# Optimization experiments

Hardware: AMD Instinct MI355X
Metric: run time of the kernel (lower is better)

Reference implementation:

```python
import jax, jax.numpy as jnp
import numpy as np

DIM = 2048
N_HEADS = 16
Q_LORA = 1536
KV_LORA = 512
NOPE = 128
ROPE = 64
V_DIM = 128
B, T = 1, 3072
EPS = 1e-6


def rmsnorm(x, w):
    var = jnp.mean(jnp.square(x), axis=-1, keepdims=True)
    return x * jax.lax.rsqrt(var + EPS) * w


def apply_rope(x, cos, sin):
    # x: (B, T, H, d); cos/sin: (T, d//2) -> broadcast (1, T, 1, d//2)
    c = cos[None, :, None, :]
    s = sin[None, :, None, :]
    x1 = x[..., 0::2]
    x2 = x[..., 1::2]
    r1 = x1 * c - x2 * s
    r2 = x1 * s + x2 * c
    return jnp.stack([r1, r2], axis=-1).reshape(x.shape)


def setup_inputs() -> dict:
    key = jax.random.key(0)
    ks = jax.random.split(key, 10)
    std = 0.02
    x = jax.random.normal(ks[0], (B, T, DIM), dtype=jnp.float32)
    # RoPE angles: position * inv_freq, shape (T, ROPE//2)
    inv_freq = 1.0 / (10000.0 ** (np.arange(0, ROPE, 2, dtype=np.float32) / ROPE))
    freqs = jnp.asarray(np.arange(T, dtype=np.float32)[:, None] * inv_freq[None, :])
    # additive causal mask (T, T)
    mask = jnp.where(jnp.tril(jnp.ones((T, T), dtype=bool)), 0.0, -jnp.inf).astype(jnp.float32)
    wq_down = jax.random.normal(ks[1], (DIM, Q_LORA), dtype=jnp.float32) * std
    q_norm_w = jnp.ones((Q_LORA,), dtype=jnp.float32)
    wq_nope = jax.random.normal(ks[2], (Q_LORA, N_HEADS * NOPE), dtype=jnp.float32) * std
    wq_rope = jax.random.normal(ks[3], (Q_LORA, N_HEADS * ROPE), dtype=jnp.float32) * std
    wkv_down = jax.random.normal(ks[4], (DIM, KV_LORA + ROPE), dtype=jnp.float32) * std
    kv_norm_w = jnp.ones((KV_LORA,), dtype=jnp.float32)
    wkv_up = jax.random.normal(ks[5], (KV_LORA, N_HEADS * (NOPE + V_DIM)), dtype=jnp.float32) * std
    wo = jax.random.normal(ks[6], (N_HEADS * V_DIM, DIM), dtype=jnp.float32) * std
    return {
        'x': x, 'freqs': freqs, 'mask': mask,
        'wq_down': wq_down, 'q_norm_w': q_norm_w, 'wq_nope': wq_nope,
        'wq_rope': wq_rope, 'wkv_down': wkv_down, 'kv_norm_w': kv_norm_w,
        'wkv_up': wkv_up, 'wo': wo,
    }


def reference(x, freqs, mask, wq_down, q_norm_w, wq_nope, wq_rope,
              wkv_down, kv_norm_w, wkv_up, wo):
    cos, sin = jnp.cos(freqs), jnp.sin(freqs)
    # Q path: down-project, RMSNorm, split nope/rope heads
    q_lat = rmsnorm(x @ wq_down, q_norm_w)                      # (B,T,Q_LORA)
    q_nope = (q_lat @ wq_nope).reshape(B, T, N_HEADS, NOPE)
    q_rope = apply_rope((q_lat @ wq_rope).reshape(B, T, N_HEADS, ROPE), cos, sin)
    q = jnp.concatenate([q_nope, q_rope], axis=-1)              # (B,T,H,192)
    # KV path: joint down-projection -> latent c_kv + raw rope key
    kvd = x @ wkv_down                                          # (B,T,KV_LORA+ROPE)
    c_kv = kvd[..., :KV_LORA]
    k_rope_raw = kvd[..., KV_LORA:]                             # (B,T,ROPE)
    k_rope = jnp.broadcast_to(k_rope_raw[:, :, None, :], (B, T, N_HEADS, ROPE))
    k_rope = apply_rope(k_rope, cos, sin)
    kv_up = (rmsnorm(c_kv, kv_norm_w) @ wkv_up).reshape(B, T, N_HEADS, NOPE + V_DIM)
    k_nope = kv_up[..., :NOPE]
    v = kv_up[..., NOPE:]                                       # (B,T,H,V_DIM)
    k = jnp.concatenate([k_nope, k_rope], axis=-1)              # (B,T,H,192)
    scale = (NOPE + ROPE) ** (-0.5)
    attn = jnp.einsum('bqhd,bkhd->bhqk', q, k) * scale + mask[None, None]
    attn = jax.nn.softmax(attn, axis=-1)                        # dropout p=0 (eval)
    out = jnp.einsum('bhqk,bkhd->bqhd', attn, v).reshape(B, T, N_HEADS * V_DIM)
    return out @ wo                                             # (B,T,DIM)
```

## Files before the change

### kernel.cpp

```cpp
#include <hip/hip_runtime.h>
#include <hip/hip_bf16.h>

typedef __bf16 bf16_t;
typedef __bf16 bf16x8 __attribute__((ext_vector_type(8)));
typedef float f32x4 __attribute__((ext_vector_type(4)));

#define T_SEQ 3072
#define DIM 2048
#define NH 16
#define QLORA 1536
#define KVLORA 512
#define NOPE 128
#define ROPE 64
#define VDIM 128
#define HD 192
#define SCALE 0.07216878364870323f
#define CHUNK 12

#define T1KV_LD 2112
#define QNR_LD 3072

__device__ inline float wave_reduce_sum(float v) {
    #pragma unroll
    for (int off = 32; off > 0; off >>= 1) v += __shfl_down(v, off);
    return v;
}

__device__ inline float block_reduce_sum_256(float v) {
    __shared__ float red[4];
    int lane = threadIdx.x & 63, w = threadIdx.x >> 6;
    v = wave_reduce_sum(v);
    if (lane == 0) red[w] = v;
    __syncthreads();
    if (threadIdx.x == 0) red[0] = red[0] + red[1] + red[2] + red[3];
    __syncthreads();
    return red[0];
}

__device__ inline void glds16(const bf16_t* g, bf16_t* l) {
    __builtin_amdgcn_global_load_lds(
        (const __attribute__((address_space(1))) unsigned int*)g,
        (__attribute__((address_space(3))) unsigned int*)l, 16, 0, 0);
}

__global__ void f2b_kernel(const float* __restrict__ in, bf16_t* __restrict__ out, int n) {
    int i = (blockIdx.x * 256 + threadIdx.x) * 4;
    if (i < n) {
        float4 v = *(const float4*)&in[i];
        bf16_t o[4] = {(bf16_t)v.x, (bf16_t)v.y, (bf16_t)v.z, (bf16_t)v.w};
        *(uint2*)&out[i] = *(const uint2*)o;
    }
}

__global__ __launch_bounds__(256) void transp_kernel(
    const float* __restrict__ in, bf16_t* __restrict__ out, int K, int N)
{
    __shared__ float tile[32][33];
    int k0 = blockIdx.y * 32, n0 = blockIdx.x * 32;
    int tx = threadIdx.x & 31, ty = threadIdx.x >> 5;
    #pragma unroll
    for (int i = 0; i < 4; ++i)
        tile[ty + i * 8][tx] = in[(size_t)(k0 + ty + i * 8) * N + n0 + tx];
    __syncthreads();
    #pragma unroll
    for (int i = 0; i < 4; ++i)
        out[(size_t)(n0 + ty + i * 8) * K + k0 + tx] = (bf16_t)tile[tx][ty + i * 8];
}

__global__ __launch_bounds__(256) void vt_transp(
    const bf16_t* __restrict__ kvu, bf16_t* __restrict__ vt)
{
    __shared__ bf16_t tile[32][34];
    int t0 = blockIdx.x * 32, d0 = blockIdx.y * 32, h = blockIdx.z;
    int tx = threadIdx.x & 31, ty = threadIdx.x >> 5;
    #pragma unroll
    for (int i = 0; i < 4; ++i)
        tile[ty + i * 8][tx] = kvu[(size_t)(t0 + ty + i * 8) * (NH * 256) + h * 256 + NOPE + d0 + tx];
    __syncthreads();
    #pragma unroll
    for (int i = 0; i < 4; ++i)
        vt[((size_t)h * VDIM + d0 + ty + i * 8) * T_SEQ + t0 + tx] = tile[tx][ty + i * 8];
}

__global__ __launch_bounds__(256) void gemm_mfma(
    const bf16_t* __restrict__ A, const bf16_t* __restrict__ Bt,
    float* __restrict__ Cf, bf16_t* __restrict__ Cb,
    int M, int N, int K, int lda, int ldb, int ldc, int writef)
{
    __shared__ __align__(16) bf16_t As[2][128 * 32];
    __shared__ __align__(16) bf16_t Bs[2][128 * 32];
    int tid = threadIdx.x;
    int w = tid >> 6, lane = tid & 63;
    int quad = lane >> 4, l16 = lane & 15;
    int bm = blockIdx.y * 128, bn = blockIdx.x * 128;
    int wm = (w & 1) * 64, wn = (w >> 1) * 64;

    int srow = tid >> 2, soff = (tid & 3) * 8;
    const bf16_t* a0 = A + (size_t)(bm + srow) * lda + soff;
    const bf16_t* a1 = A + (size_t)(bm + 64 + srow) * lda + soff;
    int br0 = bn + srow;      if (br0 >= N) br0 = N - 1;
    int br1 = bn + 64 + srow; if (br1 >= N) br1 = N - 1;
    const bf16_t* b0 = Bt + (size_t)br0 * ldb + soff;
    const bf16_t* b1 = Bt + (size_t)br1 * ldb + soff;

    f32x4 acc[4][4];
    #pragma unroll
    for (int i = 0; i < 4; ++i)
        #pragma unroll
        for (int j = 0; j < 4; ++j)
            acc[i][j] = (f32x4){0.f, 0.f, 0.f, 0.f};

    int nk = K >> 5;
    glds16(a0, &As[0][tid * 8]);
    glds16(a1, &As[0][tid * 8 + 2048]);
    glds16(b0, &Bs[0][tid * 8]);
    glds16(b1, &Bs[0][tid * 8 + 2048]);
    a0 += 32; a1 += 32; b0 += 32; b1 += 32;

    for (int t = 0; t < nk; ++t) {
        int cur = t & 1;
        if (t + 1 < nk) {
            int nxt = cur ^ 1;
            glds16(a0, &As[nxt][tid * 8]);
            glds16(a1, &As[nxt][tid * 8 + 2048]);
            glds16(b0, &Bs[nxt][tid * 8]);
            glds16(b1, &Bs[nxt][tid * 8 + 2048]);
            a0 += 32; a1 += 32; b0 += 32; b1 += 32;
            asm volatile("s_waitcnt vmcnt(4)" ::: "memory");
        } else {
            asm volatile("s_waitcnt vmcnt(0)" ::: "memory");
        }
        __builtin_amdgcn_s_barrier();
        __builtin_amdgcn_sched_barrier(0);

        bf16x8 af[4], bfr[4];
        #pragma unroll
        for (int t4 = 0; t4 < 4; ++t4) {
            af[t4]  = *(const bf16x8*)&As[cur][(wm + t4 * 16 + l16) * 32 + quad * 8];
            bfr[t4] = *(const bf16x8*)&Bs[cur][(wn + t4 * 16 + l16) * 32 + quad * 8];
        }
        #pragma unroll
        for (int i = 0; i < 4; ++i)
            #pragma unroll
            for (int j = 0; j < 4; ++j)
                acc[i][j] = __builtin_amdgcn_mfma_f32_16x16x32_bf16(af[i], bfr[j], acc[i][j], 0, 0, 0);

        __builtin_amdgcn_sched_barrier(0);
        __builtin_amdgcn_s_barrier();
    }

    #pragma unroll
    for (int i = 0; i < 4; ++i) {
        #pragma unroll
        for (int j = 0; j < 4; ++j) {
            #pragma unroll
            for (int r = 0; r < 4; ++r) {
                int row = bm + wm + i * 16 + quad * 4 + r;
                int col = bn + wn + j * 16 + l16;
                if (col < N) {
                    if (writef) Cf[(size_t)row * ldc + col] = acc[i][j][r];
                    else        Cb[(size_t)row * ldc + col] = (bf16_t)acc[i][j][r];
                }
            }
        }
    }
}

__global__ __launch_bounds__(256) void rmsnorm_rows(
    bf16_t* __restrict__ X, const float* __restrict__ w, int N, int ld)
{
    int row = blockIdx.x;
    bf16_t* x = X + (size_t)row * ld;
    float ss = 0.f;
    for (int i = threadIdx.x; i < N; i += 256) { float v = (float)x[i]; ss += v * v; }
    ss = block_reduce_sum_256(ss);
    float sc = rsqrtf(ss / (float)N + 1e-6f);
    for (int i = threadIdx.x; i < N; i += 256)
        x[i] = (bf16_t)((float)x[i] * sc * w[i]);
}

__global__ __launch_bounds__(256) void kv_post(
    const bf16_t* __restrict__ kvd, const float* __restrict__ w,
    const float* __restrict__ freqs,
    bf16_t* __restrict__ ckvn, bf16_t* __restrict__ kr)
{
    int row = blockIdx.x;
    const bf16_t* src = kvd + (size_t)row * T1KV_LD;
    float ss = 0.f;
    for (int i = threadIdx.x; i < KVLORA; i += 256) { float v = (float)src[i]; ss += v * v; }
    ss = block_reduce_sum_256(ss);
    float sc = rsqrtf(ss / (float)KVLORA + 1e-6f);
    for (int i = threadIdx.x; i < KVLORA; i += 256)
        ckvn[(size_t)row * KVLORA + i] = (bf16_t)((float)src[i] * sc * w[i]);
    if (threadIdx.x < 32) {
        int i = threadIdx.x;
        float f = freqs[row * 32 + i];
        float c = cosf(f), s = sinf(f);
        float x1 = (float)src[KVLORA + 2 * i], x2 = (float)src[KVLORA + 2 * i + 1];
        kr[(size_t)row * ROPE + 2 * i]     = (bf16_t)(x1 * c - x2 * s);
        kr[(size_t)row * ROPE + 2 * i + 1] = (bf16_t)(x1 * s + x2 * c);
    }
}

__global__ void rope_q(bf16_t* __restrict__ qr, const float* __restrict__ freqs) {
    int idx = blockIdx.x * 256 + threadIdx.x;
    if (idx >= T_SEQ * NH * 32) return;
    int t = idx >> 9;
    int rem = idx & 511;
    int h = rem >> 5;
    int i = rem & 31;
    float f = freqs[t * 32 + i];
    float c = cosf(f), s = sinf(f);
    bf16_t* p = qr + (size_t)t * QNR_LD + h * ROPE + 2 * i;
    float x1 = (float)p[0], x2 = (float)p[1];
    p[0] = (bf16_t)(x1 * c - x2 * s);
    p[1] = (bf16_t)(x1 * s + x2 * c);
}

#define P_STRIDE 72
__device__ inline int slot_base(int qt, int h) {
    int b = qt / CHUNK;
    return h * 120 + qt + 6 * b * (b - 1) + (qt - CHUNK * b) * b;
}
__global__ __launch_bounds__(256) void attn_v8(
    const bf16_t* __restrict__ QNR,
    const bf16_t* __restrict__ KVU, const bf16_t* __restrict__ KR,
    const bf16_t* __restrict__ Vt,
    bf16_t* __restrict__ Opart, float* __restrict__ lpart)
{
    __shared__ __align__(16) bf16_t Kn[64 * 128];
    __shared__ __align__(16) bf16_t Kr[64 * 64];
    __shared__ __align__(16) bf16_t Vs[128 * 64];
    __shared__ __align__(16) bf16_t Ps[4][16 * P_STRIDE];

    int qt = blockIdx.x, cx = blockIdx.y, h = blockIdx.z;
    if (cx > qt / CHUNK) return;
    int slot = slot_base(qt, h) + cx;
    int kt0 = cx * CHUNK;
    int kt1 = min(qt + 1, kt0 + CHUNK);

    int tid = threadIdx.x;
    int w = tid >> 6, lane = tid & 63;
    int quad = lane >> 4, l16 = lane & 15;
    int qbase = qt * 64;

    bf16x8 qf[6];
    {
        int qrow = qbase + w * 16 + l16;
        #pragma unroll
        for (int kk = 0; kk < 4; ++kk)
            qf[kk] = *(const bf16x8*)&QNR[(size_t)qrow * QNR_LD + h * NOPE + kk * 32 + quad * 8];
        #pragma unroll
        for (int kk = 4; kk < 6; ++kk)
            qf[kk] = *(const bf16x8*)&QNR[(size_t)qrow * QNR_LD + (NH * NOPE) + h * ROPE + (kk - 4) * 32 + quad * 8];
    }

    int l4 = lane >> 4, l3 = lane >> 3;
    const bf16_t* kn_e = KVU + (size_t)(kt0 * 64 + w * 16 + l4) * (NH * 256) + h * 256 + ((lane & 15) ^ l4) * 8;
    const bf16_t* kn_o = KVU + (size_t)(kt0 * 64 + w * 16 + l4) * (NH * 256) + h * 256 + ((lane & 15) ^ (4 + l4)) * 8;
    const bf16_t* krp  = KR  + (size_t)(kt0 * 64 + w * 16 + l3) * ROPE + ((lane & 7) ^ l3) * 8;
    const bf16_t* vp   = Vt  + ((size_t)h * VDIM + w * 32 + l3) * T_SEQ + kt0 * 64 + ((lane & 7) ^ l3) * 8;

    bf16x8 ones;
    #pragma unroll
    for (int i = 0; i < 8; ++i) ones[i] = (bf16_t)1.0f;

    f32x4 o[8];
    #pragma unroll
    for (int nt = 0; nt < 8; ++nt) o[nt] = (f32x4){0.f, 0.f, 0.f, 0.f};
    f32x4 lacc = (f32x4){0.f, 0.f, 0.f, 0.f};

    for (int kt = kt0; kt < kt1; ++kt) {
        int kbase = kt * 64;
        #pragma unroll
        for (int i = 0; i < 4; ++i)
            glds16(((i & 1) ? kn_o : kn_e) + (size_t)i * 4 * (NH * 256), &Kn[(w * 4 + i) * 512]);
        #pragma unroll
        for (int i = 0; i < 2; ++i)
            glds16(krp + (size_t)i * 8 * ROPE, &Kr[(w * 2 + i) * 512]);
        #pragma unroll
        for (int i = 0; i < 4; ++i)
            glds16(vp + (size_t)i * 8 * T_SEQ, &Vs[(w * 4 + i) * 512]);
        kn_e += (size_t)64 * NH * 256;
        kn_o += (size_t)64 * NH * 256;
        krp  += 64 * ROPE;
        vp   += 64;
        __syncthreads();

        f32x4 S[4];
        #pragma unroll
        for (int c = 0; c < 4; ++c) S[c] = (f32x4){0.f, 0.f, 0.f, 0.f};
        #pragma unroll
        for (int kk = 0; kk < 4; ++kk) {
            #pragma unroll
            for (int c = 0; c < 4; ++c) {
                bf16x8 kf = *(const bf16x8*)&Kn[(c * 16 + l16) * 128 + (((kk * 4 + quad) ^ (l16 & 7)) * 8)];
                S[c] = __builtin_amdgcn_mfma_f32_16x16x32_bf16(qf[kk], kf, S[c], 0, 0, 0);
            }
        }
        #pragma unroll
        for (int kk = 4; kk < 6; ++kk) {
            #pragma unroll
            for (int c = 0; c < 4; ++c) {
                bf16x8 kf = *(const bf16x8*)&Kr[(c * 16 + l16) * 64 + ((((kk - 4) * 4 + quad) ^ (l16 & 7)) * 8)];
                S[c] = __builtin_amdgcn_mfma_f32_16x16x32_bf16(qf[kk], kf, S[c], 0, 0, 0);
            }
        }

        #pragma unroll
        for (int c = 0; c < 4; ++c) {
            #pragma unroll
            for (int j = 0; j < 4; ++j) {
                int col = kbase + c * 16 + l16;
                int grow = qbase + w * 16 + quad * 4 + j;
                float p = (col <= grow) ? __expf(S[c][j] * SCALE) : 0.f;
                Ps[w][(quad * 4 + j) * P_STRIDE + c * 16 + l16] = (bf16_t)p;
            }
        }
        __asm__ volatile("s_waitcnt lgkmcnt(0)" ::: "memory");

        bf16x8 pf0 = *(const bf16x8*)&Ps[w][l16 * P_STRIDE + quad * 8];
        bf16x8 pf1 = *(const bf16x8*)&Ps[w][l16 * P_STRIDE + 32 + quad * 8];
        lacc = __builtin_amdgcn_mfma_f32_16x16x32_bf16(pf0, ones, lacc, 0, 0, 0);
        lacc = __builtin_amdgcn_mfma_f32_16x16x32_bf16(pf1, ones, lacc, 0, 0, 0);

        #pragma unroll
        for (int kk2 = 0; kk2 < 2; ++kk2) {
            bf16x8 pf = kk2 ? pf1 : pf0;
            #pragma unroll
            for (int nt = 0; nt < 8; ++nt) {
                bf16x8 vf = *(const bf16x8*)&Vs[(nt * 16 + l16) * 64 + (((kk2 * 4 + quad) ^ (l16 & 7)) * 8)];
                o[nt] = __builtin_amdgcn_mfma_f32_16x16x32_bf16(pf, vf, o[nt], 0, 0, 0);
            }
        }
        __syncthreads();
    }

    #pragma unroll
    for (int nt = 0; nt < 8; ++nt)
        #pragma unroll
        for (int j = 0; j < 4; ++j)
            Opart[(size_t)slot * 8192 + (w * 16 + quad * 4 + j) * 128 + nt * 16 + l16] = (bf16_t)o[nt][j];
    if (l16 == 0) {
        #pragma unroll
        for (int j = 0; j < 4; ++j)
            lpart[slot * 64 + w * 16 + quad * 4 + j] = lacc[j];
    }
}

__global__ __launch_bounds__(256) void attn_combine(
    const bf16_t* __restrict__ Opart, const float* __restrict__ lpart,
    bf16_t* __restrict__ AO)
{
    int qt = blockIdx.x, h = blockIdx.y;
    int nch = qt / CHUNK + 1;
    int base = slot_base(qt, h);
    int r = threadIdx.x >> 2, c0 = (threadIdx.x & 3) * 32;

    float acc[32];
    #pragma unroll
    for (int i = 0; i < 32; ++i) acc[i] = 0.f;
    float lsum = 0.f;
    for (int ch = 0; ch < nch; ++ch) {
        int slot = base + ch;
        const bf16_t* p = &Opart[(size_t)slot * 8192 + r * 128 + c0];
        #pragma unroll
        for (int v = 0; v < 4; ++v) {
            bf16x8 u = *(const bf16x8*)&p[v * 8];
            #pragma unroll
            for (int e = 0; e < 8; ++e) acc[v * 8 + e] += (float)u[e];
        }
        lsum += lpart[slot * 64 + r];
    }
    float inv = 1.0f / lsum;
    bf16_t* dst = AO + (size_t)(qt * 64 + r) * (NH * VDIM) + h * VDIM + c0;
    #pragma unroll
    for (int v = 0; v < 4; ++v) {
        bf16_t tmp[8];
        #pragma unroll
        for (int e = 0; e < 8; ++e) tmp[e] = (bf16_t)(acc[v * 8 + e] * inv);
        *(uint4*)&dst[v * 8] = *(const uint4*)tmp;
    }
}

extern "C" void kernel_launch(void* const* d_in, const int* in_sizes, int n_in,
                              void* d_out, int out_size, void* d_ws, size_t ws_size,
                              hipStream_t stream) {
    const float* x        = (const float*)d_in[0];
    const float* freqs    = (const float*)d_in[1];
    const float* wq_down  = (const float*)d_in[3];
    const float* q_norm_w = (const float*)d_in[4];
    const float* wq_nope  = (const float*)d_in[5];
    const float* wq_rope  = (const float*)d_in[6];
    const float* wkv_down = (const float*)d_in[7];
    const float* kv_norm_w= (const float*)d_in[8];
    const float* wkv_up   = (const float*)d_in[9];
    const float* wo       = (const float*)d_in[10];
    float* out = (float*)d_out;

    bf16_t* ws = (bf16_t*)d_ws;
    bf16_t* xb     = ws;
    bf16_t* wqd_t  = xb     + 6291456;
    bf16_t* wkvd_t = wqd_t  + 3145728;
    bf16_t* wqn_t  = wkvd_t + 1179648;
    bf16_t* wqr_t  = wqn_t  + 3145728;
    bf16_t* wkvu_t = wqr_t  + 1572864;
    bf16_t* t1kv   = wkvu_t + 2097152;
    bf16_t* ckvn   = t1kv   + 6488064;
    bf16_t* Opart  = ws;
    float*  lpart  = (float*)(ws + 15728640);
    bf16_t* ao     = ws + 15728640 + 245760;
    bf16_t* wo_t   = ws    + 25493504;
    bf16_t* kr     = wo_t  + 4194304;
    bf16_t* qnr    = kr    + 196608;
    bf16_t* kvu    = qnr   + 9437184;
    bf16_t* vt     = kvu   + 12582912;

    f2b_kernel<<<T_SEQ * DIM / 4 / 256, 256, 0, stream>>>(x, xb, T_SEQ * DIM);
    transp_kernel<<<dim3(QLORA / 32, DIM / 32), 256, 0, stream>>>(wq_down, wqd_t, DIM, QLORA);
    transp_kernel<<<dim3((KVLORA + ROPE) / 32, DIM / 32), 256, 0, stream>>>(wkv_down, wkvd_t, DIM, KVLORA + ROPE);
    transp_kernel<<<dim3(NH * NOPE / 32, QLORA / 32), 256, 0, stream>>>(wq_nope, wqn_t, QLORA, NH * NOPE);
    transp_kernel<<<dim3(NH * ROPE / 32, QLORA / 32), 256, 0, stream>>>(wq_rope, wqr_t, QLORA, NH * ROPE);
    transp_kernel<<<dim3(NH * 256 / 32, KVLORA / 32), 256, 0, stream>>>(wkv_up, wkvu_t, KVLORA, NH * 256);
    transp_kernel<<<dim3(DIM / 32, DIM / 32), 256, 0, stream>>>(wo, wo_t, DIM, DIM);

    gemm_mfma<<<dim3(17, T_SEQ / 128), 256, 0, stream>>>(
        xb, wqd_t, nullptr, t1kv, T_SEQ, 2112, DIM, DIM, DIM, T1KV_LD, 0);

    rmsnorm_rows<<<T_SEQ, 256, 0, stream>>>(t1kv, q_norm_w, QLORA, T1KV_LD);
    kv_post<<<T_SEQ, 256, 0, stream>>>(t1kv + QLORA, kv_norm_w, freqs, ckvn, kr);

    gemm_mfma<<<dim3(24, T_SEQ / 128), 256, 0, stream>>>(
        t1kv, wqn_t, nullptr, qnr, T_SEQ, 3072, QLORA, T1KV_LD, QLORA, QNR_LD, 0);
    rope_q<<<(T_SEQ * NH * 32 + 255) / 256, 256, 0, stream>>>(qnr + NH * NOPE, freqs);

    gemm_mfma<<<dim3(NH * 256 / 128, T_SEQ / 128), 256, 0, stream>>>(
        ckvn, wkvu_t, nullptr, kvu, T_SEQ, NH * 256, KVLORA, KVLORA, KVLORA, NH * 256, 0);

    vt_transp<<<dim3(T_SEQ / 32, VDIM / 32, NH), 256, 0, stream>>>(kvu, vt);

    attn_v8<<<dim3(T_SEQ / 64, 4, NH), 256, 0, stream>>>(qnr, kvu, kr, vt, Opart, lpart);
    attn_combine<<<dim3(T_SEQ / 64, NH), 256, 0, stream>>>(Opart, lpart, ao);

    gemm_mfma<<<dim3(DIM / 128, T_SEQ / 128), 256, 0, stream>>>(
        ao, wo_t, out, nullptr, T_SEQ, DIM, DIM, DIM, DIM, DIM, 1);
}
```

Baseline: 476.8 us.

## Double query tile per attention block and double-buffer K/V loads

The split-K attention kernel now uses 512 threads and covers 128 query rows per block instead of 64. Each loaded K/V tile therefore serves twice as many queries, which halves global K/V traffic. K, rope-K and V tiles are double-buffered in LDS, and the next tile's async global-to-LDS loads are issued before computing on the current tile, with explicit vmcnt waits. Slot indexing and the combine kernel are adjusted for the new tile and chunk layout. The trade-off is doubled LDS use, fewer blocks, and more masked-out work per diagonal tile.

```diff
diff --git a/kernel.cpp b/kernel.cpp
--- a/kernel.cpp
+++ b/kernel.cpp
@@ -147,6 +147,7 @@
 
         __builtin_amdgcn_sched_barrier(0);
         __builtin_amdgcn_s_barrier();
+        __builtin_amdgcn_sched_barrier(0);
     }
 
     #pragma unroll
@@ -218,31 +219,29 @@
 }
 
 #define P_STRIDE 72
-__device__ inline int slot_base(int qt, int h) {
-    int b = qt / CHUNK;
-    return h * 120 + qt + 6 * b * (b - 1) + (qt - CHUNK * b) * b;
-}
-__global__ __launch_bounds__(256) void attn_v8(
+__global__ __launch_bounds__(512) void attn_v9(
     const bf16_t* __restrict__ QNR,
     const bf16_t* __restrict__ KVU, const bf16_t* __restrict__ KR,
     const bf16_t* __restrict__ Vt,
     bf16_t* __restrict__ Opart, float* __restrict__ lpart)
 {
-    __shared__ __align__(16) bf16_t Kn[64 * 128];
-    __shared__ __align__(16) bf16_t Kr[64 * 64];
-    __shared__ __align__(16) bf16_t Vs[128 * 64];
-    __shared__ __align__(16) bf16_t Ps[4][16 * P_STRIDE];
-
-    int qt = blockIdx.x, cx = blockIdx.y, h = blockIdx.z;
-    if (cx > qt / CHUNK) return;
-    int slot = slot_base(qt, h) + cx;
+    __shared__ __align__(16) bf16_t Kn[2][64 * 128];
+    __shared__ __align__(16) bf16_t Kr[2][64 * 64];
+    __shared__ __align__(16) bf16_t Vs[2][128 * 64];
+    __shared__ __align__(16) bf16_t Ps[8][16 * P_STRIDE];
+
+    int qt2 = blockIdx.x, cx = blockIdx.y, h = blockIdx.z;
+    int ktmax = 2 * qt2 + 2;
     int kt0 = cx * CHUNK;
-    int kt1 = min(qt + 1, kt0 + CHUNK);
+    if (kt0 >= ktmax) return;
+    int kt1 = min(ktmax, kt0 + CHUNK);
+    int g = qt2 / 6, r6 = qt2 - g * 6;
+    int slot = h * 60 + 3 * g * (g + 1) + r6 * (g + 1) + cx;
 
     int tid = threadIdx.x;
     int w = tid >> 6, lane = tid & 63;
     int quad = lane >> 4, l16 = lane & 15;
-    int qbase = qt * 64;
+    int qbase = qt2 * 128;
 
     bf16x8 qf[6];
     {
@@ -256,10 +255,10 @@
     }
 
     int l4 = lane >> 4, l3 = lane >> 3;
-    const bf16_t* kn_e = KVU + (size_t)(kt0 * 64 + w * 16 + l4) * (NH * 256) + h * 256 + ((lane & 15) ^ l4) * 8;
-    const bf16_t* kn_o = KVU + (size_t)(kt0 * 64 + w * 16 + l4) * (NH * 256) + h * 256 + ((lane & 15) ^ (4 + l4)) * 8;
-    const bf16_t* krp  = KR  + (size_t)(kt0 * 64 + w * 16 + l3) * ROPE + ((lane & 7) ^ l3) * 8;
-    const bf16_t* vp   = Vt  + ((size_t)h * VDIM + w * 32 + l3) * T_SEQ + kt0 * 64 + ((lane & 7) ^ l3) * 8;
+    const bf16_t* kn0 = KVU + (size_t)(kt0 * 64 + w * 8 + l4) * (NH * 256) + h * 256 + ((lane & 15) ^ l4) * 8;
+    const bf16_t* kn1 = KVU + (size_t)(kt0 * 64 + w * 8 + 4 + l4) * (NH * 256) + h * 256 + ((lane & 15) ^ (4 + l4)) * 8;
+    const bf16_t* krp = KR + (size_t)(kt0 * 64 + w * 8 + l3) * ROPE + ((lane & 7) ^ l3) * 8;
+    const bf16_t* vp  = Vt + ((size_t)h * VDIM + w * 16 + l3) * T_SEQ + kt0 * 64 + ((lane & 7) ^ l3) * 8;
 
     bf16x8 ones;
     #pragma unroll
@@ -270,22 +269,32 @@
     for (int nt = 0; nt < 8; ++nt) o[nt] = (f32x4){0.f, 0.f, 0.f, 0.f};
     f32x4 lacc = (f32x4){0.f, 0.f, 0.f, 0.f};
 
+    glds16(kn0,               &Kn[0][w * 1024]);
+    glds16(kn1,               &Kn[0][w * 1024 + 512]);
+    glds16(krp,               &Kr[0][w * 512]);
+    glds16(vp,                &Vs[0][w * 1024]);
+    glds16(vp + 8 * T_SEQ,    &Vs[0][w * 1024 + 512]);
+    kn0 += (size_t)64 * NH * 256; kn1 += (size_t)64 * NH * 256;
+    krp += 64 * ROPE; vp += 64;
+
     for (int kt = kt0; kt < kt1; ++kt) {
         int kbase = kt * 64;
-        #pragma unroll
-        for (int i = 0; i < 4; ++i)
-            glds16(((i & 1) ? kn_o : kn_e) + (size_t)i * 4 * (NH * 256), &Kn[(w * 4 + i) * 512]);
-        #pragma unroll
-        for (int i = 0; i < 2; ++i)
-            glds16(krp + (size_t)i * 8 * ROPE, &Kr[(w * 2 + i) * 512]);
-        #pragma unroll
-        for (int i = 0; i < 4; ++i)
-            glds16(vp + (size_t)i * 8 * T_SEQ, &Vs[(w * 4 + i) * 512]);
-        kn_e += (size_t)64 * NH * 256;
-        kn_o += (size_t)64 * NH * 256;
-        krp  += 64 * ROPE;
-        vp   += 64;
-        __syncthreads();
+        int cur = (kt - kt0) & 1;
+        if (kt + 1 < kt1) {
+            int nxt = cur ^ 1;
+            glds16(kn0,            &Kn[nxt][w * 1024]);
+            glds16(kn1,            &Kn[nxt][w * 1024 + 512]);
+            glds16(krp,            &Kr[nxt][w * 512]);
+            glds16(vp,             &Vs[nxt][w * 1024]);
+            glds16(vp + 8 * T_SEQ, &Vs[nxt][w * 1024 + 512]);
+            kn0 += (size_t)64 * NH * 256; kn1 += (size_t)64 * NH * 256;
+            krp += 64 * ROPE; vp += 64;
+            asm volatile("s_waitcnt vmcnt(5)" ::: "memory");
+        } else {
+            asm volatile("s_waitcnt vmcnt(0)" ::: "memory");
+        }
+        __builtin_amdgcn_s_barrier();
+        __builtin_amdgcn_sched_barrier(0);
 
         f32x4 S[4];
         #pragma unroll
@@ -294,7 +303,7 @@
         for (int kk = 0; kk < 4; ++kk) {
             #pragma unroll
             for (int c = 0; c < 4; ++c) {
-                bf16x8 kf = *(const bf16x8*)&Kn[(c * 16 + l16) * 128 + (((kk * 4 + quad) ^ (l16 & 7)) * 8)];
+                bf16x8 kf = *(const bf16x8*)&Kn[cur][(c * 16 + l16) * 128 + (((kk * 4 + quad) ^ (l16 & 7)) * 8)];
                 S[c] = __builtin_amdgcn_mfma_f32_16x16x32_bf16(qf[kk], kf, S[c], 0, 0, 0);
             }
         }
@@ -302,7 +311,7 @@
         for (int kk = 4; kk < 6; ++kk) {
             #pragma unroll
             for (int c = 0; c < 4; ++c) {
-                bf16x8 kf = *(const bf16x8*)&Kr[(c * 16 + l16) * 64 + ((((kk - 4) * 4 + quad) ^ (l16 & 7)) * 8)];
+                bf16x8 kf = *(const bf16x8*)&Kr[cur][(c * 16 + l16) * 64 + ((((kk - 4) * 4 + quad) ^ (l16 & 7)) * 8)];
                 S[c] = __builtin_amdgcn_mfma_f32_16x16x32_bf16(qf[kk], kf, S[c], 0, 0, 0);
             }
         }
@@ -329,32 +338,35 @@
             bf16x8 pf = kk2 ? pf1 : pf0;
             #pragma unroll
             for (int nt = 0; nt < 8; ++nt) {
-                bf16x8 vf = *(const bf16x8*)&Vs[(nt * 16 + l16) * 64 + (((kk2 * 4 + quad) ^ (l16 & 7)) * 8)];
+                bf16x8 vf = *(const bf16x8*)&Vs[cur][(nt * 16 + l16) * 64 + (((kk2 * 4 + quad) ^ (l16 & 7)) * 8)];
                 o[nt] = __builtin_amdgcn_mfma_f32_16x16x32_bf16(pf, vf, o[nt], 0, 0, 0);
             }
         }
-        __syncthreads();
+        __builtin_amdgcn_sched_barrier(0);
+        __builtin_amdgcn_s_barrier();
+        __builtin_amdgcn_sched_barrier(0);
     }
 
     #pragma unroll
     for (int nt = 0; nt < 8; ++nt)
         #pragma unroll
         for (int j = 0; j < 4; ++j)
-            Opart[(size_t)slot * 8192 + (w * 16 + quad * 4 + j) * 128 + nt * 16 + l16] = (bf16_t)o[nt][j];
+            Opart[(size_t)slot * 16384 + (w * 16 + quad * 4 + j) * 128 + nt * 16 + l16] = (bf16_t)o[nt][j];
     if (l16 == 0) {
         #pragma unroll
         for (int j = 0; j < 4; ++j)
-            lpart[slot * 64 + w * 16 + quad * 4 + j] = lacc[j];
-    }
-}
-
-__global__ __launch_bounds__(256) void attn_combine(
+            lpart[slot * 128 + w * 16 + quad * 4 + j] = lacc[j];
+    }
+}
+
+__global__ __launch_bounds__(512) void attn_combine(
     const bf16_t* __restrict__ Opart, const float* __restrict__ lpart,
     bf16_t* __restrict__ AO)
 {
-    int qt = blockIdx.x, h = blockIdx.y;
-    int nch = qt / CHUNK + 1;
-    int base = slot_base(qt, h);
+    int qt2 = blockIdx.x, h = blockIdx.y;
+    int g = qt2 / 6, r6 = qt2 - g * 6;
+    int nch = g + 1;
+    int base = h * 60 + 3 * g * (g + 1) + r6 * (g + 1);
     int r = threadIdx.x >> 2, c0 = (threadIdx.x & 3) * 32;
 
     float acc[32];
@@ -363,17 +375,17 @@
     float lsum = 0.f;
     for (int ch = 0; ch < nch; ++ch) {
         int slot = base + ch;
-        const bf16_t* p = &Opart[(size_t)slot * 8192 + r * 128 + c0];
+        const bf16_t* p = &Opart[(size_t)slot * 16384 + r * 128 + c0];
         #pragma unroll
         for (int v = 0; v < 4; ++v) {
             bf16x8 u = *(const bf16x8*)&p[v * 8];
             #pragma unroll
             for (int e = 0; e < 8; ++e) acc[v * 8 + e] += (float)u[e];
         }
-        lsum += lpart[slot * 64 + r];
+        lsum += lpart[slot * 128 + r];
     }
     float inv = 1.0f / lsum;
-    bf16_t* dst = AO + (size_t)(qt * 64 + r) * (NH * VDIM) + h * VDIM + c0;
+    bf16_t* dst = AO + (size_t)(qt2 * 128 + r) * (NH * VDIM) + h * VDIM + c0;
     #pragma unroll
     for (int v = 0; v < 4; ++v) {
         bf16_t tmp[8];
@@ -439,8 +451,8 @@
 
     vt_transp<<<dim3(T_SEQ / 32, VDIM / 32, NH), 256, 0, stream>>>(kvu, vt);
 
-    attn_v8<<<dim3(T_SEQ / 64, 4, NH), 256, 0, stream>>>(qnr, kvu, kr, vt, Opart, lpart);
-    attn_combine<<<dim3(T_SEQ / 64, NH), 256, 0, stream>>>(Opart, lpart, ao);
+    attn_v9<<<dim3(T_SEQ / 128, 4, NH), 512, 0, stream>>>(qnr, kvu, kr, vt, Opart, lpart);
+    attn_combine<<<dim3(T_SEQ / 128, NH), 512, 0, stream>>>(Opart, lpart, ao);
 
     gemm_mfma<<<dim3(DIM / 128, T_SEQ / 128), 256, 0, stream>>>(
         ao, wo_t, out, nullptr, T_SEQ, DIM, DIM, DIM, DIM, DIM, 1);
```

Result: slower. 529.1 us (+11.0%).

## Process two query tiles per attention block to reuse K/V tiles

Applied to the files above, without the earlier changes.

The attention kernel now handles 128 query rows per block, as two 64-row sub-tiles sharing each loaded K and V tile, which halves global-to-LDS K/V traffic per query. Slot indexing, partial buffers and the combine kernel are reworked for 128-row slots, and the combine now uses 512 threads. The cost is double the accumulator and Q-fragment registers, bounded by launch_bounds(256,2), and fewer blocks for the causal split. A sched_barrier is also added after the GEMM loop barrier.

```diff
diff --git a/kernel.cpp b/kernel.cpp
--- a/kernel.cpp
+++ b/kernel.cpp
@@ -147,6 +147,7 @@
 
         __builtin_amdgcn_sched_barrier(0);
         __builtin_amdgcn_s_barrier();
+        __builtin_amdgcn_sched_barrier(0);
     }
 
     #pragma unroll
@@ -218,11 +219,7 @@
 }
 
 #define P_STRIDE 72
-__device__ inline int slot_base(int qt, int h) {
-    int b = qt / CHUNK;
-    return h * 120 + qt + 6 * b * (b - 1) + (qt - CHUNK * b) * b;
-}
-__global__ __launch_bounds__(256) void attn_v8(
+__global__ __launch_bounds__(256, 2) void attn_v10(
     const bf16_t* __restrict__ QNR,
     const bf16_t* __restrict__ KVU, const bf16_t* __restrict__ KR,
     const bf16_t* __restrict__ Vt,
@@ -231,28 +228,31 @@
     __shared__ __align__(16) bf16_t Kn[64 * 128];
     __shared__ __align__(16) bf16_t Kr[64 * 64];
     __shared__ __align__(16) bf16_t Vs[128 * 64];
-    __shared__ __align__(16) bf16_t Ps[4][16 * P_STRIDE];
-
-    int qt = blockIdx.x, cx = blockIdx.y, h = blockIdx.z;
-    if (cx > qt / CHUNK) return;
-    int slot = slot_base(qt, h) + cx;
+    __shared__ __align__(16) bf16_t Ps[4][32 * P_STRIDE];
+
+    int qt2 = blockIdx.x, cx = blockIdx.y, h = blockIdx.z;
+    int ktmax = 2 * qt2 + 2;
     int kt0 = cx * CHUNK;
-    int kt1 = min(qt + 1, kt0 + CHUNK);
+    if (kt0 >= ktmax) return;
+    int kt1 = min(ktmax, kt0 + CHUNK);
+    int g = qt2 / 6, r6 = qt2 - g * 6;
+    int slot = h * 60 + 3 * g * (g + 1) + r6 * (g + 1) + cx;
 
     int tid = threadIdx.x;
     int w = tid >> 6, lane = tid & 63;
     int quad = lane >> 4, l16 = lane & 15;
-    int qbase = qt * 64;
-
-    bf16x8 qf[6];
-    {
-        int qrow = qbase + w * 16 + l16;
+    int qbase = qt2 * 128;
+
+    bf16x8 qf[2][6];
+    #pragma unroll
+    for (int qs = 0; qs < 2; ++qs) {
+        int qrow = qbase + qs * 64 + w * 16 + l16;
         #pragma unroll
         for (int kk = 0; kk < 4; ++kk)
-            qf[kk] = *(const bf16x8*)&QNR[(size_t)qrow * QNR_LD + h * NOPE + kk * 32 + quad * 8];
+            qf[qs][kk] = *(const bf16x8*)&QNR[(size_t)qrow * QNR_LD + h * NOPE + kk * 32 + quad * 8];
         #pragma unroll
         for (int kk = 4; kk < 6; ++kk)
-            qf[kk] = *(const bf16x8*)&QNR[(size_t)qrow * QNR_LD + (NH * NOPE) + h * ROPE + (kk - 4) * 32 + quad * 8];
+            qf[qs][kk] = *(const bf16x8*)&QNR[(size_t)qrow * QNR_LD + (NH * NOPE) + h * ROPE + (kk - 4) * 32 + quad * 8];
     }
 
     int l4 = lane >> 4, l3 = lane >> 3;
@@ -265,10 +265,14 @@
     #pragma unroll
     for (int i = 0; i < 8; ++i) ones[i] = (bf16_t)1.0f;
 
-    f32x4 o[8];
-    #pragma unroll
-    for (int nt = 0; nt < 8; ++nt) o[nt] = (f32x4){0.f, 0.f, 0.f, 0.f};
-    f32x4 lacc = (f32x4){0.f, 0.f, 0.f, 0.f};
+    f32x4 o[2][8];
+    #pragma unroll
+    for (int qs = 0; qs < 2; ++qs)
+        #pragma unroll
+        for (int nt = 0; nt < 8; ++nt) o[qs][nt] = (f32x4){0.f, 0.f, 0.f, 0.f};
+    f32x4 lacc[2];
+    lacc[0] = (f32x4){0.f, 0.f, 0.f, 0.f};
+    lacc[1] = (f32x4){0.f, 0.f, 0.f, 0.f};
 
     for (int kt = kt0; kt < kt1; ++kt) {
         int kbase = kt * 64;
@@ -287,15 +291,18 @@
         vp   += 64;
         __syncthreads();
 
-        f32x4 S[4];
-        #pragma unroll
-        for (int c = 0; c < 4; ++c) S[c] = (f32x4){0.f, 0.f, 0.f, 0.f};
+        f32x4 S[2][4];
+        #pragma unroll
+        for (int qs = 0; qs < 2; ++qs)
+            #pragma unroll
+            for (int c = 0; c < 4; ++c) S[qs][c] = (f32x4){0.f, 0.f, 0.f, 0.f};
         #pragma unroll
         for (int kk = 0; kk < 4; ++kk) {
             #pragma unroll
             for (int c = 0; c < 4; ++c) {
                 bf16x8 kf = *(const bf16x8*)&Kn[(c * 16 + l16) * 128 + (((kk * 4 + quad) ^ (l16 & 7)) * 8)];
-                S[c] = __builtin_amdgcn_mfma_f32_16x16x32_bf16(qf[kk], kf, S[c], 0, 0, 0);
+                S[0][c] = __builtin_amdgcn_mfma_f32_16x16x32_bf16(qf[0][kk], kf, S[0][c], 0, 0, 0);
+                S[1][c] = __builtin_amdgcn_mfma_f32_16x16x32_bf16(qf[1][kk], kf, S[1][c], 0, 0, 0);
             }
         }
         #pragma unroll
@@ -303,58 +310,70 @@
             #pragma unroll
             for (int c = 0; c < 4; ++c) {
                 bf16x8 kf = *(const bf16x8*)&Kr[(c * 16 + l16) * 64 + ((((kk - 4) * 4 + quad) ^ (l16 & 7)) * 8)];
-                S[c] = __builtin_amdgcn_mfma_f32_16x16x32_bf16(qf[kk], kf, S[c], 0, 0, 0);
+                S[0][c] = __builtin_amdgcn_mfma_f32_16x16x32_bf16(qf[0][kk], kf, S[0][c], 0, 0, 0);
+                S[1][c] = __builtin_amdgcn_mfma_f32_16x16x32_bf16(qf[1][kk], kf, S[1][c], 0, 0, 0);
             }
         }
 
         #pragma unroll
-        for (int c = 0; c < 4; ++c) {
-            #pragma unroll
-            for (int j = 0; j < 4; ++j) {
-                int col = kbase + c * 16 + l16;
-                int grow = qbase + w * 16 + quad * 4 + j;
-                float p = (col <= grow) ? __expf(S[c][j] * SCALE) : 0.f;
-                Ps[w][(quad * 4 + j) * P_STRIDE + c * 16 + l16] = (bf16_t)p;
+        for (int qs = 0; qs < 2; ++qs) {
+            #pragma unroll
+            for (int c = 0; c < 4; ++c) {
+                #pragma unroll
+                for (int j = 0; j < 4; ++j) {
+                    int col = kbase + c * 16 + l16;
+                    int grow = qbase + qs * 64 + w * 16 + quad * 4 + j;
+                    float p = (col <= grow) ? __expf(S[qs][c][j] * SCALE) : 0.f;
+                    Ps[w][(qs * 16 + quad * 4 + j) * P_STRIDE + c * 16 + l16] = (bf16_t)p;
+                }
             }
         }
         __asm__ volatile("s_waitcnt lgkmcnt(0)" ::: "memory");
 
-        bf16x8 pf0 = *(const bf16x8*)&Ps[w][l16 * P_STRIDE + quad * 8];
-        bf16x8 pf1 = *(const bf16x8*)&Ps[w][l16 * P_STRIDE + 32 + quad * 8];
-        lacc = __builtin_amdgcn_mfma_f32_16x16x32_bf16(pf0, ones, lacc, 0, 0, 0);
-        lacc = __builtin_amdgcn_mfma_f32_16x16x32_bf16(pf1, ones, lacc, 0, 0, 0);
+        bf16x8 pf[2][2];
+        #pragma unroll
+        for (int qs = 0; qs < 2; ++qs) {
+            pf[qs][0] = *(const bf16x8*)&Ps[w][(qs * 16 + l16) * P_STRIDE + quad * 8];
+            pf[qs][1] = *(const bf16x8*)&Ps[w][(qs * 16 + l16) * P_STRIDE + 32 + quad * 8];
+            lacc[qs] = __builtin_amdgcn_mfma_f32_16x16x32_bf16(pf[qs][0], ones, lacc[qs], 0, 0, 0);
+            lacc[qs] = __builtin_amdgcn_mfma_f32_16x16x32_bf16(pf[qs][1], ones, lacc[qs], 0, 0, 0);
+        }
 
         #pragma unroll
         for (int kk2 = 0; kk2 < 2; ++kk2) {
-            bf16x8 pf = kk2 ? pf1 : pf0;
             #pragma unroll
             for (int nt = 0; nt < 8; ++nt) {
                 bf16x8 vf = *(const bf16x8*)&Vs[(nt * 16 + l16) * 64 + (((kk2 * 4 + quad) ^ (l16 & 7)) * 8)];
-                o[nt] = __builtin_amdgcn_mfma_f32_16x16x32_bf16(pf, vf, o[nt], 0, 0, 0);
+                o[0][nt] = __builtin_amdgcn_mfma_f32_16x16x32_bf16(pf[0][kk2], vf, o[0][nt], 0, 0, 0);
+                o[1][nt] = __builtin_amdgcn_mfma_f32_16x16x32_bf16(pf[1][kk2], vf, o[1][nt], 0, 0, 0);
             }
         }
         __syncthreads();
     }
 
     #pragma unroll
-    for (int nt = 0; nt < 8; ++nt)
-        #pragma unroll
-        for (int j = 0; j < 4; ++j)
-            Opart[(size_t)slot * 8192 + (w * 16 + quad * 4 + j) * 128 + nt * 16 + l16] = (bf16_t)o[nt][j];
-    if (l16 == 0) {
-        #pragma unroll
-        for (int j = 0; j < 4; ++j)
-            lpart[slot * 64 + w * 16 + quad * 4 + j] = lacc[j];
-    }
-}
-
-__global__ __launch_bounds__(256) void attn_combine(
+    for (int qs = 0; qs < 2; ++qs) {
+        #pragma unroll
+        for (int nt = 0; nt < 8; ++nt)
+            #pragma unroll
+            for (int j = 0; j < 4; ++j)
+                Opart[(size_t)slot * 16384 + (qs * 64 + w * 16 + quad * 4 + j) * 128 + nt * 16 + l16] = (bf16_t)o[qs][nt][j];
+        if (l16 == 0) {
+            #pragma unroll
+            for (int j = 0; j < 4; ++j)
+                lpart[slot * 128 + qs * 64 + w * 16 + quad * 4 + j] = lacc[qs][j];
+        }
+    }
+}
+
+__global__ __launch_bounds__(512) void attn_combine(
     const bf16_t* __restrict__ Opart, const float* __restrict__ lpart,
     bf16_t* __restrict__ AO)
 {
-    int qt = blockIdx.x, h = blockIdx.y;
-    int nch = qt / CHUNK + 1;
-    int base = slot_base(qt, h);
+    int qt2 = blockIdx.x, h = blockIdx.y;
+    int g = qt2 / 6, r6 = qt2 - g * 6;
+    int nch = g + 1;
+    int base = h * 60 + 3 * g * (g + 1) + r6 * (g + 1);
     int r = threadIdx.x >> 2, c0 = (threadIdx.x & 3) * 32;
 
     float acc[32];
@@ -363,17 +382,17 @@
     float lsum = 0.f;
     for (int ch = 0; ch < nch; ++ch) {
         int slot = base + ch;
-        const bf16_t* p = &Opart[(size_t)slot * 8192 + r * 128 + c0];
+        const bf16_t* p = &Opart[(size_t)slot * 16384 + r * 128 + c0];
         #pragma unroll
         for (int v = 0; v < 4; ++v) {
             bf16x8 u = *(const bf16x8*)&p[v * 8];
             #pragma unroll
             for (int e = 0; e < 8; ++e) acc[v * 8 + e] += (float)u[e];
         }
-        lsum += lpart[slot * 64 + r];
+        lsum += lpart[slot * 128 + r];
     }
     float inv = 1.0f / lsum;
-    bf16_t* dst = AO + (size_t)(qt * 64 + r) * (NH * VDIM) + h * VDIM + c0;
+    bf16_t* dst = AO + (size_t)(qt2 * 128 + r) * (NH * VDIM) + h * VDIM + c0;
     #pragma unroll
     for (int v = 0; v < 4; ++v) {
         bf16_t tmp[8];
@@ -439,8 +458,8 @@
 
     vt_transp<<<dim3(T_SEQ / 32, VDIM / 32, NH), 256, 0, stream>>>(kvu, vt);
 
-    attn_v8<<<dim3(T_SEQ / 64, 4, NH), 256, 0, stream>>>(qnr, kvu, kr, vt, Opart, lpart);
-    attn_combine<<<dim3(T_SEQ / 64, NH), 256, 0, stream>>>(Opart, lpart, ao);
+    attn_v10<<<dim3(T_SEQ / 128, 4, NH), 256, 0, stream>>>(qnr, kvu, kr, vt, Opart, lpart);
+    attn_combine<<<dim3(T_SEQ / 128, NH), 512, 0, stream>>>(Opart, lpart, ao);
 
     gemm_mfma<<<dim3(DIM / 128, T_SEQ / 128), 256, 0, stream>>>(
         ao, wo_t, out, nullptr, T_SEQ, DIM, DIM, DIM, DIM, DIM, 1);
```

After: 483.4 us. Within noise of the previous version (+1.4%).
